# Performance work log

Measured on AMD Instinct MI355X. Metric: run time of the kernel, lower is better.

The kernel has to match this reference:

```python
import jax, jax.numpy as jnp
import numpy as np

NUM_GROUPS = 8
NUM_HEADS = 4
EPS = 1e-5


def group_norm(x, w, b):
    # x: [B, C, H, W]; normalize over (C/G, H, W) within each of G groups
    B, C, H, W = x.shape
    xg = x.reshape(B, NUM_GROUPS, C // NUM_GROUPS, H, W)
    mean = xg.mean(axis=(2, 3, 4), keepdims=True)
    var = xg.var(axis=(2, 3, 4), keepdims=True)
    xn = ((xg - mean) * jax.lax.rsqrt(var + EPS)).reshape(B, C, H, W)
    return xn * w[None, :, None, None] + b[None, :, None, None]


def setup_inputs() -> dict:
    key = jax.random.key(0)
    ks = jax.random.split(key, 7)
    B, C, H, W = 4, 256, 64, 64
    x = jax.random.normal(ks[0], (B, C, H, W), dtype=jnp.float32)
    gn_w = jax.random.normal(ks[1], (C,), dtype=jnp.float32) * 0.1 + 1.0
    gn_b = jax.random.normal(ks[2], (C,), dtype=jnp.float32) * 0.1
    qkv_w = jax.random.normal(ks[3], (3 * C, C), dtype=jnp.float32) / np.sqrt(C)
    qkv_b = jax.random.normal(ks[4], (3 * C,), dtype=jnp.float32) * 0.02
    proj_w = jax.random.normal(ks[5], (C, C), dtype=jnp.float32) / np.sqrt(C)
    proj_b = jax.random.normal(ks[6], (C,), dtype=jnp.float32) * 0.02
    return {"x": x, "gn_w": gn_w, "gn_b": gn_b, "qkv_w": qkv_w,
            "qkv_b": qkv_b, "proj_w": proj_w, "proj_b": proj_b}


def reference(x, gn_w, gn_b, qkv_w, qkv_b, proj_w, proj_b):
    B, C, H, W = x.shape
    nh = NUM_HEADS
    hd = C // nh
    scale = hd ** -0.5
    N = H * W

    h = group_norm(x, gn_w, gn_b)
    # 1x1 conv == channel matmul: [B, 3C, H, W]
    qkv = jnp.einsum('oc,bchw->bohw', qkv_w, h) + qkv_b[None, :, None, None]
    qkv = qkv.reshape(B, 3, nh, hd, N)  # matches torch .view(B,3,nh,hd,HW)
    q, k, v = qkv[:, 0], qkv[:, 1], qkv[:, 2]  # each [B, nh, hd, N]

    attn = jnp.einsum('bhdn,bhdm->bhnm', q, k) * scale  # [B, nh, N, N]
    attn = jax.nn.softmax(attn, axis=-1)
    out = jnp.einsum('bhnm,bhdm->bhdn', attn, v)  # [B, nh, hd, N]
    out = out.reshape(B, C, H, W)

    proj = jnp.einsum('oc,bchw->bohw', proj_w, out) + proj_b[None, :, None, None]
    return x + proj
```

## Files before the change

kernel.cpp:

```cpp
#include <hip/hip_runtime.h>
#include <hip/hip_bf16.h>

#define BB   4
#define CC   256
#define NN   4096
#define NH   4
#define HD   64
#define NG   8
#define GSZ  32
#define EPSV 1e-5f
#define SCALE_L2E 0.18033688f

typedef __bf16 bf16x8 __attribute__((ext_vector_type(8)));
typedef float  f32x4  __attribute__((ext_vector_type(4)));
typedef short  short4v __attribute__((ext_vector_type(4)));

#define MFMA16(a, b, c)  __builtin_amdgcn_mfma_f32_16x16x32_bf16((a), (b), (c), 0, 0, 0)
#define MFMAPV(a, b, c)  __builtin_amdgcn_mfma_f32_16x16x16bf16_1k((a), (b), (c), 0, 0, 0)

#if __has_builtin(__builtin_amdgcn_exp2f)
#define EXP2F __builtin_amdgcn_exp2f
#else
#define EXP2F exp2f
#endif

__device__ inline unsigned short f2bf(float f) {
    unsigned int u = __float_as_uint(f);
    u += 0x7fffu + ((u >> 16) & 1u);
    return (unsigned short)(u >> 16);
}

__device__ __forceinline__ short4v pk4(const f32x4& p) {
    alignas(8) unsigned int u[2];
    u[0] = __builtin_amdgcn_perm(__float_as_uint(p[1]), __float_as_uint(p[0]), 0x07060302u);
    u[1] = __builtin_amdgcn_perm(__float_as_uint(p[3]), __float_as_uint(p[2]), 0x07060302u);
    return *reinterpret_cast<short4v*>(u);
}

__device__ __forceinline__ void async_ld16(void* lds, const void* g) {
    __builtin_amdgcn_global_load_lds(
        (const __attribute__((address_space(1))) unsigned int*)g,
        (__attribute__((address_space(3))) unsigned int*)lds, 16, 0, 0);
}

__global__ void k_prep(const float* __restrict__ x, float* __restrict__ stats,
                       const float* __restrict__ wq, const float* __restrict__ wp,
                       unsigned short* __restrict__ oq, unsigned short* __restrict__ op) {
    int blk = blockIdx.x;
    int t = threadIdx.x;
    if (blk >= 256) {
        int i = (blk - 256) * 256 + t;
        if (i < 3 * CC * CC) oq[i] = f2bf(wq[i]);
        if (i < CC * CC)     op[i] = f2bf(wp[i]);
        return;
    }
    int b = blk >> 6, g = (blk >> 3) & 7, s = blk & 7;
    const float* p = x + ((size_t)(b * CC + g * GSZ)) * NN + s * 16384;
    float s0 = 0.f, s1 = 0.f;
    #pragma unroll
    for (int i = 0; i < 64; ++i) { float v = p[i * 256 + t]; s0 += v; s1 += v * v; }
    #pragma unroll
    for (int m = 1; m <= 32; m <<= 1) { s0 += __shfl_xor(s0, m); s1 += __shfl_xor(s1, m); }
    __shared__ float ls[8];
    int w = t >> 6;
    if ((t & 63) == 0) { ls[w * 2] = s0; ls[w * 2 + 1] = s1; }
    __syncthreads();
    if (t == 0) {
        float a0 = ls[0] + ls[2] + ls[4] + ls[6];
        float a1 = ls[1] + ls[3] + ls[5] + ls[7];
        atomicAdd(&stats[(b * NG + g) * 2 + 0], a0);
        atomicAdd(&stats[(b * NG + g) * 2 + 1], a1);
    }
}

__global__ void k_gnapply(const float* __restrict__ x, const float* __restrict__ gw,
                          const float* __restrict__ gb, const float* __restrict__ stats,
                          unsigned short* __restrict__ ht) {
    int b = blockIdx.z, ct = blockIdx.y, nt = blockIdx.x;
    int c0 = ct * 32, n0 = nt * 64;
    int t = threadIdx.x;
    __shared__ float tile[32][65];
    const float* xp = x + ((size_t)(b * CC + c0)) * NN + n0;
    int cl = t >> 6, nl = t & 63;
    #pragma unroll
    for (int p = 0; p < 8; ++p)
        tile[p * 4 + cl][nl] = xp[(size_t)(p * 4 + cl) * NN + nl];
    float sum = stats[(b * NG + ct) * 2 + 0];
    float ssq = stats[(b * NG + ct) * 2 + 1];
    float mean = sum * (1.0f / 131072.0f);
    float var  = ssq * (1.0f / 131072.0f) - mean * mean;
    float inv  = rsqrtf(var + EPSV);
    __syncthreads();
    int nw = t >> 2, ci = (t & 3) * 8;
    alignas(16) unsigned short o8[8];
    #pragma unroll
    for (int j = 0; j < 8; ++j) {
        int c = c0 + ci + j;
        float v = (tile[ci + j][nw] - mean) * inv * gw[c] + gb[c];
        o8[j] = f2bf(v);
    }
    *reinterpret_cast<uint4*>(ht + ((size_t)(b * NN + n0 + nw)) * CC + c0 + ci) =
        *reinterpret_cast<const uint4*>(o8);
}

__global__ void __launch_bounds__(256)
k_qkv(const unsigned short* __restrict__ ht, const unsigned short* __restrict__ wq,
      const float* __restrict__ qb,
      unsigned short* __restrict__ qt, unsigned short* __restrict__ kt,
      unsigned short* __restrict__ vt) {
    int bx = blockIdx.x, by = blockIdx.y;
    int t = threadIdx.x, wave = t >> 6, lane = t & 63;
    int l15 = lane & 15, quad = lane >> 4;
    int wm = wave >> 1, wn = wave & 1;

    __shared__ alignas(16) unsigned char At[2][8192];
    __shared__ alignas(16) unsigned char Bt[2][8192];

    const char* Ag = (const char*)wq + (size_t)by * 65536;
    const char* Bg = (const char*)ht + (size_t)bx * 65536;
    int row0 = t >> 2, slot = t & 3;
    size_t a0 = (size_t)row0 * 512 + slot * 16;
    size_t a1 = a0 + 64 * 512;
    unsigned int dst0 = wave * 1024;

    auto stage = [&](int buf, int kk) {
        size_t ko = (size_t)kk * 64;
        async_ld16(At[buf] + dst0,        Ag + a0 + ko);
        async_ld16(At[buf] + 4096 + dst0, Ag + a1 + ko);
        async_ld16(Bt[buf] + dst0,        Bg + a0 + ko);
        async_ld16(Bt[buf] + 4096 + dst0, Bg + a1 + ko);
    };

    f32x4 acc[4][4];
    #pragma unroll
    for (int i = 0; i < 4; ++i)
        #pragma unroll
        for (int j = 0; j < 4; ++j) acc[i][j] = (f32x4){0.f, 0.f, 0.f, 0.f};

    stage(0, 0);
    __syncthreads();

    for (int kk = 0; kk < 8; ++kk) {
        int cur = kk & 1;
        if (kk < 7) stage(cur ^ 1, kk + 1);
        bf16x8 af[4], bf[4];
        #pragma unroll
        for (int f = 0; f < 4; ++f) {
            af[f] = *reinterpret_cast<const bf16x8*>(At[cur] + (wm * 64 + f * 16 + l15) * 64 + quad * 16);
            bf[f] = *reinterpret_cast<const bf16x8*>(Bt[cur] + (wn * 64 + f * 16 + l15) * 64 + quad * 16);
        }
        #pragma unroll
        for (int fm = 0; fm < 4; ++fm)
            #pragma unroll
            for (int fn = 0; fn < 4; ++fn)
                acc[fm][fn] = MFMA16(af[fm], bf[fn], acc[fm][fn]);
        __syncthreads();
    }

    int s = by >> 1;
    int nn0 = bx * 128;
    int b = nn0 >> 12, nbase = nn0 & 4095;
    #pragma unroll
    for (int fm = 0; fm < 4; ++fm) {
        int o = by * 128 + wm * 64 + fm * 16 + quad * 4;
        int h = (o >> 6) & 3, d0 = o & 63;
        float bias[4];
        #pragma unroll
        for (int r = 0; r < 4; ++r) bias[r] = qb[o + r];
        #pragma unroll
        for (int fn = 0; fn < 4; ++fn) {
            int n = nbase + wn * 64 + fn * 16 + l15;
            if (s == 0) {
                alignas(8) unsigned short o4[4];
                #pragma unroll
                for (int r = 0; r < 4; ++r) o4[r] = f2bf((acc[fm][fn][r] + bias[r]) * SCALE_L2E);
                *reinterpret_cast<uint2*>(qt + (((size_t)(b * NH + h) * NN) + n) * HD + d0) =
                    *reinterpret_cast<const uint2*>(o4);
            } else if (s == 1) {
                alignas(8) unsigned short o4[4];
                #pragma unroll
                for (int r = 0; r < 4; ++r) o4[r] = f2bf(acc[fm][fn][r] + bias[r]);
                *reinterpret_cast<uint2*>(kt + (((size_t)(b * NH + h) * NN) + n) * HD + d0) =
                    *reinterpret_cast<const uint2*>(o4);
            } else {
                #pragma unroll
                for (int r = 0; r < 4; ++r)
                    vt[((size_t)(b * NH + h) * HD + d0 + r) * NN + n] = f2bf(acc[fm][fn][r] + bias[r]);
            }
        }
    }
}

__global__ void __launch_bounds__(256, 4)
k_attn(const unsigned short* __restrict__ qt, const unsigned short* __restrict__ kt,
       const unsigned short* __restrict__ vt,
       unsigned short* __restrict__ op0, unsigned short* __restrict__ op1,
       float* __restrict__ lip) {
    int bh = blockIdx.y;
    int split = blockIdx.z;
    int t = threadIdx.x, wave = t >> 6, lane = t & 63;
    int l15 = lane & 15, quad = lane >> 4;
    int qbase = blockIdx.x * 128 + wave * 32;
    int kbase = split * 2048;
    const unsigned short* qp = qt + (size_t)bh * NN * HD;
    const unsigned short* kp = kt + (size_t)bh * NN * HD;
    const unsigned short* vp = vt + (size_t)bh * HD * NN;

    __shared__ alignas(16) unsigned char kbuf[2][8192];
    __shared__ alignas(16) unsigned char vbuf[2][8192];

    int lr8 = lane >> 3, lc8 = lane & 7;
    int swz = lc8 ^ lr8;
    const char* ksrc = (const char*)kp + (size_t)(kbase + wave * 16 + lr8) * 128 + swz * 16;
    const char* vsrc = (const char*)vp + (size_t)(wave * 16 + lr8) * 8192 + (size_t)kbase * 2 + swz * 16;
    unsigned int dstw = wave * 2048;

    auto stage = [&](int buf) {
        async_ld16(kbuf[buf] + dstw,        ksrc);
        async_ld16(kbuf[buf] + dstw + 1024, ksrc + 1024);
        ksrc += 8192;
        async_ld16(vbuf[buf] + dstw,        vsrc);
        async_ld16(vbuf[buf] + dstw + 1024, vsrc + 8 * 8192);
        vsrc += 128;
    };

    bf16x8 qaA0 = *reinterpret_cast<const bf16x8*>(qp + (size_t)(qbase + l15) * HD + quad * 8);
    bf16x8 qaA1 = *reinterpret_cast<const bf16x8*>(qp + (size_t)(qbase + l15) * HD + 32 + quad * 8);
    bf16x8 qaB0 = *reinterpret_cast<const bf16x8*>(qp + (size_t)(qbase + 16 + l15) * HD + quad * 8);
    bf16x8 qaB1 = *reinterpret_cast<const bf16x8*>(qp + (size_t)(qbase + 16 + l15) * HD + 32 + quad * 8);

    f32x4 OA[4], OB[4];
    #pragma unroll
    for (int i = 0; i < 4; ++i) { OA[i] = (f32x4){0.f, 0.f, 0.f, 0.f}; OB[i] = (f32x4){0.f, 0.f, 0.f, 0.f}; }
    float liA = 0.f, liB = 0.f;

    int sx = l15 & 7;

    auto compute = [&](const unsigned char* kb, const unsigned char* vbb) {
        #pragma unroll
        for (int s = 0; s < 2; ++s) {
            int r0 = (s * 32 + l15) * 128;
            bf16x8 k00 = *reinterpret_cast<const bf16x8*>(kb + r0 + ((quad ^ sx) * 16));
            bf16x8 k01 = *reinterpret_cast<const bf16x8*>(kb + r0 + (((quad + 4) ^ sx) * 16));
            bf16x8 k10 = *reinterpret_cast<const bf16x8*>(kb + r0 + 2048 + ((quad ^ sx) * 16));
            bf16x8 k11 = *reinterpret_cast<const bf16x8*>(kb + r0 + 2048 + (((quad + 4) ^ sx) * 16));
            f32x4 sA0 = {0.f,0.f,0.f,0.f}, sA1 = {0.f,0.f,0.f,0.f};
            f32x4 sB0 = {0.f,0.f,0.f,0.f}, sB1 = {0.f,0.f,0.f,0.f};
            sA0 = MFMA16(k00, qaA0, sA0);  sA0 = MFMA16(k01, qaA1, sA0);
            sA1 = MFMA16(k10, qaA0, sA1);  sA1 = MFMA16(k11, qaA1, sA1);
            sB0 = MFMA16(k00, qaB0, sB0);  sB0 = MFMA16(k01, qaB1, sB0);
            sB1 = MFMA16(k10, qaB0, sB1);  sB1 = MFMA16(k11, qaB1, sB1);

            f32x4 pA0, pA1, pB0, pB1;
            #pragma unroll
            for (int r = 0; r < 4; ++r) {
                pA0[r] = EXP2F(sA0[r]);  pA1[r] = EXP2F(sA1[r]);
                pB0[r] = EXP2F(sB0[r]);  pB1[r] = EXP2F(sB1[r]);
            }
            liA += (pA0[0] + pA0[1] + pA0[2] + pA0[3]) + (pA1[0] + pA1[1] + pA1[2] + pA1[3]);
            liB += (pB0[0] + pB0[1] + pB0[2] + pB0[3]) + (pB1[0] + pB1[1] + pB1[2] + pB1[3]);

            short4v fA0 = pk4(pA0), fA1 = pk4(pA1), fB0 = pk4(pB0), fB1 = pk4(pB1);

            #pragma unroll
            for (int dc = 0; dc < 4; ++dc) {
                int c0 = ((s * 4 + (quad >> 1)) ^ sx) * 16 + (quad & 1) * 8;
                int c1 = ((s * 4 + 2 + (quad >> 1)) ^ sx) * 16 + (quad & 1) * 8;
                const unsigned char* vrow = vbb + (dc * 16 + l15) * 128;
                short4v v0 = *reinterpret_cast<const short4v*>(vrow + c0);
                short4v v1 = *reinterpret_cast<const short4v*>(vrow + c1);
                OA[dc] = MFMAPV(fA0, v0, OA[dc]);
                OA[dc] = MFMAPV(fA1, v1, OA[dc]);
                OB[dc] = MFMAPV(fB0, v0, OB[dc]);
                OB[dc] = MFMAPV(fB1, v1, OB[dc]);
            }
        }
    };

    stage(0);
    __syncthreads();

    for (int p = 0; p < 16; ++p) {
        stage(1);
        compute(kbuf[0], vbuf[0]);
        __syncthreads();
        if (p < 15) stage(0);
        compute(kbuf[1], vbuf[1]);
        __syncthreads();
    }

    liA += __shfl_xor(liA, 16);  liA += __shfl_xor(liA, 32);
    liB += __shfl_xor(liB, 16);  liB += __shfl_xor(liB, 32);

    unsigned short* op = split ? op1 : op0;
    int b = bh >> 2, h = bh & 3;
    #pragma unroll
    for (int dc = 0; dc < 4; ++dc) {
        #pragma unroll
        for (int r = 0; r < 4; ++r) {
            int qA = qbase + quad * 4 + r;
            op[((size_t)(b * NN) + qA) * CC + h * HD + dc * 16 + l15]      = f2bf(OA[dc][r]);
            op[((size_t)(b * NN) + qA + 16) * CC + h * HD + dc * 16 + l15] = f2bf(OB[dc][r]);
        }
    }
    float* lp = lip + (size_t)split * (16 * NN) + (size_t)bh * NN + qbase;
    if (quad == 0)      lp[l15]      = liA;
    else if (quad == 1) lp[16 + l15] = liB;
}

__global__ void __launch_bounds__(256)
k_comb(unsigned short* ao, const unsigned short* __restrict__ p1, const float* __restrict__ lip) {
    int g = blockIdx.x * 256 + threadIdx.x;
    int d8 = g & 7;
    int h  = (g >> 3) & 3;
    int n  = (g >> 5) & 4095;
    int b  = g >> 17;
    int bh = b * 4 + h;
    float li0 = lip[(size_t)bh * NN + n];
    float li1 = lip[(size_t)16 * NN + (size_t)bh * NN + n];
    float inv = 1.0f / (li0 + li1);
    size_t idx = ((size_t)(b * NN) + n) * CC + h * HD + d8 * 8;
    uint4 u0 = *reinterpret_cast<const uint4*>(ao + idx);
    uint4 u1 = *reinterpret_cast<const uint4*>(p1 + idx);
    const unsigned short* a0 = reinterpret_cast<const unsigned short*>(&u0);
    const unsigned short* a1 = reinterpret_cast<const unsigned short*>(&u1);
    alignas(16) unsigned short o8[8];
    #pragma unroll
    for (int i = 0; i < 8; ++i) {
        float f0 = __uint_as_float((unsigned)a0[i] << 16);
        float f1 = __uint_as_float((unsigned)a1[i] << 16);
        o8[i] = f2bf((f0 + f1) * inv);
    }
    *reinterpret_cast<uint4*>(ao + idx) = *reinterpret_cast<const uint4*>(o8);
}

__global__ void __launch_bounds__(256)
k_proj(const unsigned short* __restrict__ ao, const unsigned short* __restrict__ wp,
       const float* __restrict__ pb, const float* __restrict__ x,
       float* __restrict__ out) {
    int bx = blockIdx.x, by = blockIdx.y;
    int t = threadIdx.x, wave = t >> 6, lane = t & 63;
    int l15 = lane & 15, quad = lane >> 4;
    int wm = wave >> 1, wn = wave & 1;

    __shared__ alignas(16) unsigned char At[2][4096];
    __shared__ alignas(16) unsigned char Bt[2][4096];

    const char* Ag = (const char*)wp + (size_t)by * 32768;
    const char* Bg = (const char*)ao + (size_t)bx * 32768;
    int row0 = t >> 2, slot = t & 3;
    size_t a0 = (size_t)row0 * 512 + slot * 16;
    unsigned int dst0 = wave * 1024;

    auto stage = [&](int buf, int kk) {
        size_t ko = (size_t)kk * 64;
        async_ld16(At[buf] + dst0, Ag + a0 + ko);
        async_ld16(Bt[buf] + dst0, Bg + a0 + ko);
    };

    f32x4 acc[2][2];
    #pragma unroll
    for (int i = 0; i < 2; ++i)
        #pragma unroll
        for (int j = 0; j < 2; ++j) acc[i][j] = (f32x4){0.f, 0.f, 0.f, 0.f};

    stage(0, 0);
    __syncthreads();

    for (int kk = 0; kk < 8; ++kk) {
        int cur = kk & 1;
        if (kk < 7) stage(cur ^ 1, kk + 1);
        bf16x8 af[2], bf[2];
        #pragma unroll
        for (int f = 0; f < 2; ++f) {
            af[f] = *reinterpret_cast<const bf16x8*>(At[cur] + (wm * 32 + f * 16 + l15) * 64 + quad * 16);
            bf[f] = *reinterpret_cast<const bf16x8*>(Bt[cur] + (wn * 32 + f * 16 + l15) * 64 + quad * 16);
        }
        #pragma unroll
        for (int fm = 0; fm < 2; ++fm)
            #pragma unroll
            for (int fn = 0; fn < 2; ++fn)
                acc[fm][fn] = MFMA16(af[fm], bf[fn], acc[fm][fn]);
        __syncthreads();
    }

    int nn0 = bx * 64;
    int b = nn0 >> 12, nbase = nn0 & 4095;
    #pragma unroll
    for (int fm = 0; fm < 2; ++fm) {
        int o = by * 64 + wm * 32 + fm * 16 + quad * 4;
        float bias[4];
        #pragma unroll
        for (int r = 0; r < 4; ++r) bias[r] = pb[o + r];
        #pragma unroll
        for (int fn = 0; fn < 2; ++fn) {
            int n = nbase + wn * 32 + fn * 16 + l15;
            #pragma unroll
            for (int r = 0; r < 4; ++r) {
                size_t idx = ((size_t)(b * CC + o + r)) * NN + n;
                out[idx] = acc[fm][fn][r] + bias[r] + x[idx];
            }
        }
    }
}

extern "C" void kernel_launch(void* const* d_in, const int* in_sizes, int n_in,
                              void* d_out, int out_size, void* d_ws, size_t ws_size,
                              hipStream_t stream) {
    const float* x     = (const float*)d_in[0];
    const float* gw    = (const float*)d_in[1];
    const float* gb    = (const float*)d_in[2];
    const float* qkvw  = (const float*)d_in[3];
    const float* qkvb  = (const float*)d_in[4];
    const float* projw = (const float*)d_in[5];
    const float* projb = (const float*)d_in[6];
    float* out = (float*)d_out;

    char* w = (char*)d_ws;
    size_t off = 0;
    unsigned short* ht = (unsigned short*)(w + off); off += (size_t)BB * NN * CC * 2;
    unsigned short* qt = (unsigned short*)(w + off); off += (size_t)BB * NH * NN * HD * 2;
    unsigned short* kt = (unsigned short*)(w + off); off += (size_t)BB * NH * NN * HD * 2;
    unsigned short* vt = (unsigned short*)(w + off); off += (size_t)BB * NH * HD * NN * 2;
    unsigned short* ao = (unsigned short*)(w + off); off += (size_t)BB * NN * CC * 2;
    unsigned short* wqb = (unsigned short*)(w + off); off += (size_t)3 * CC * CC * 2;
    unsigned short* wpb = (unsigned short*)(w + off); off += (size_t)CC * CC * 2;
    float* stats = (float*)(w + off); off += BB * NG * 2 * sizeof(float);
    float* lip   = (float*)(w + off); off += (size_t)2 * 16 * NN * sizeof(float);

    hipMemsetAsync(stats, 0, BB * NG * 2 * sizeof(float), stream);
    k_prep<<<1024, 256, 0, stream>>>(x, stats, qkvw, projw, wqb, wpb);
    k_gnapply<<<dim3(NN / 64, CC / 32, BB), 256, 0, stream>>>(x, gw, gb, stats, ht);
    k_qkv<<<dim3(BB * NN / 128, 6), 256, 0, stream>>>(ht, wqb, qkvb, qt, kt, vt);
    k_attn<<<dim3(NN / 128, BB * NH, 2), 256, 0, stream>>>(qt, kt, vt, ao, ht, lip);
    k_comb<<<2048, 256, 0, stream>>>(ao, ht, lip);
    k_proj<<<dim3(BB * NN / 64, CC / 64), 256, 0, stream>>>(ao, wpb, projb, x, out);
}
```

Before: 199.2 us.

## Fuse split-attention combine into projection GEMM and batch QK MFMAs before exp

Removes the separate k_comb kernel. The projection kernel now loads both partial attention outputs from global memory, sums them, scales by the inverse softmax denominator and writes the bf16 result into shared memory as its B operand. This saves a kernel launch and one full read-write pass over the attention output, but each of the CC/64 column blocks now redoes the combine and reads two inputs instead of one. The attention inner loop also issues all QK MFMAs for both sub-steps before the exponentials, giving the scheduler more independent MFMA work at the cost of more live registers.

Result: no change. 200.2 us (+0.5%).

```diff
diff --git a/kernel.cpp b/kernel.cpp
--- a/kernel.cpp
+++ b/kernel.cpp
@@ -237,6 +237,7 @@
     int sx = l15 & 7;
 
     auto compute = [&](const unsigned char* kb, const unsigned char* vbb) {
+        f32x4 sA0[2], sA1[2], sB0[2], sB1[2];
         #pragma unroll
         for (int s = 0; s < 2; ++s) {
             int r0 = (s * 32 + l15) * 128;
@@ -244,18 +245,20 @@
             bf16x8 k01 = *reinterpret_cast<const bf16x8*>(kb + r0 + (((quad + 4) ^ sx) * 16));
             bf16x8 k10 = *reinterpret_cast<const bf16x8*>(kb + r0 + 2048 + ((quad ^ sx) * 16));
             bf16x8 k11 = *reinterpret_cast<const bf16x8*>(kb + r0 + 2048 + (((quad + 4) ^ sx) * 16));
-            f32x4 sA0 = {0.f,0.f,0.f,0.f}, sA1 = {0.f,0.f,0.f,0.f};
-            f32x4 sB0 = {0.f,0.f,0.f,0.f}, sB1 = {0.f,0.f,0.f,0.f};
-            sA0 = MFMA16(k00, qaA0, sA0);  sA0 = MFMA16(k01, qaA1, sA0);
-            sA1 = MFMA16(k10, qaA0, sA1);  sA1 = MFMA16(k11, qaA1, sA1);
-            sB0 = MFMA16(k00, qaB0, sB0);  sB0 = MFMA16(k01, qaB1, sB0);
-            sB1 = MFMA16(k10, qaB0, sB1);  sB1 = MFMA16(k11, qaB1, sB1);
-
+            sA0[s] = (f32x4){0.f,0.f,0.f,0.f};  sA1[s] = (f32x4){0.f,0.f,0.f,0.f};
+            sB0[s] = (f32x4){0.f,0.f,0.f,0.f};  sB1[s] = (f32x4){0.f,0.f,0.f,0.f};
+            sA0[s] = MFMA16(k00, qaA0, sA0[s]);  sA0[s] = MFMA16(k01, qaA1, sA0[s]);
+            sA1[s] = MFMA16(k10, qaA0, sA1[s]);  sA1[s] = MFMA16(k11, qaA1, sA1[s]);
+            sB0[s] = MFMA16(k00, qaB0, sB0[s]);  sB0[s] = MFMA16(k01, qaB1, sB0[s]);
+            sB1[s] = MFMA16(k10, qaB0, sB1[s]);  sB1[s] = MFMA16(k11, qaB1, sB1[s]);
+        }
+        #pragma unroll
+        for (int s = 0; s < 2; ++s) {
             f32x4 pA0, pA1, pB0, pB1;
             #pragma unroll
             for (int r = 0; r < 4; ++r) {
-                pA0[r] = EXP2F(sA0[r]);  pA1[r] = EXP2F(sA1[r]);
-                pB0[r] = EXP2F(sB0[r]);  pB1[r] = EXP2F(sB1[r]);
+                pA0[r] = EXP2F(sA0[s][r]);  pA1[r] = EXP2F(sA1[s][r]);
+                pB0[r] = EXP2F(sB0[s][r]);  pB1[r] = EXP2F(sB1[s][r]);
             }
             liA += (pA0[0] + pA0[1] + pA0[2] + pA0[3]) + (pA1[0] + pA1[1] + pA1[2] + pA1[3]);
             liB += (pB0[0] + pB0[1] + pB0[2] + pB0[3]) + (pB1[0] + pB1[1] + pB1[2] + pB1[3]);
@@ -309,35 +312,10 @@
 }
 
 __global__ void __launch_bounds__(256)
-k_comb(unsigned short* ao, const unsigned short* __restrict__ p1, const float* __restrict__ lip) {
-    int g = blockIdx.x * 256 + threadIdx.x;
-    int d8 = g & 7;
-    int h  = (g >> 3) & 3;
-    int n  = (g >> 5) & 4095;
-    int b  = g >> 17;
-    int bh = b * 4 + h;
-    float li0 = lip[(size_t)bh * NN + n];
-    float li1 = lip[(size_t)16 * NN + (size_t)bh * NN + n];
-    float inv = 1.0f / (li0 + li1);
-    size_t idx = ((size_t)(b * NN) + n) * CC + h * HD + d8 * 8;
-    uint4 u0 = *reinterpret_cast<const uint4*>(ao + idx);
-    uint4 u1 = *reinterpret_cast<const uint4*>(p1 + idx);
-    const unsigned short* a0 = reinterpret_cast<const unsigned short*>(&u0);
-    const unsigned short* a1 = reinterpret_cast<const unsigned short*>(&u1);
-    alignas(16) unsigned short o8[8];
-    #pragma unroll
-    for (int i = 0; i < 8; ++i) {
-        float f0 = __uint_as_float((unsigned)a0[i] << 16);
-        float f1 = __uint_as_float((unsigned)a1[i] << 16);
-        o8[i] = f2bf((f0 + f1) * inv);
-    }
-    *reinterpret_cast<uint4*>(ao + idx) = *reinterpret_cast<const uint4*>(o8);
-}
-
-__global__ void __launch_bounds__(256)
-k_proj(const unsigned short* __restrict__ ao, const unsigned short* __restrict__ wp,
-       const float* __restrict__ pb, const float* __restrict__ x,
-       float* __restrict__ out) {
+k_proj(const unsigned short* __restrict__ p0, const unsigned short* __restrict__ p1,
+       const float* __restrict__ lip,
+       const unsigned short* __restrict__ wp, const float* __restrict__ pb,
+       const float* __restrict__ x, float* __restrict__ out) {
     int bx = blockIdx.x, by = blockIdx.y;
     int t = threadIdx.x, wave = t >> 6, lane = t & 63;
     int l15 = lane & 15, quad = lane >> 4;
@@ -347,15 +325,44 @@
     __shared__ alignas(16) unsigned char Bt[2][4096];
 
     const char* Ag = (const char*)wp + (size_t)by * 32768;
-    const char* Bg = (const char*)ao + (size_t)bx * 32768;
     int row0 = t >> 2, slot = t & 3;
     size_t a0 = (size_t)row0 * 512 + slot * 16;
     unsigned int dst0 = wave * 1024;
 
-    auto stage = [&](int buf, int kk) {
-        size_t ko = (size_t)kk * 64;
-        async_ld16(At[buf] + dst0, Ag + a0 + ko);
-        async_ld16(Bt[buf] + dst0, Bg + a0 + ko);
+    int nn0 = bx * 64;
+    int b = nn0 >> 12, nbase = nn0 & 4095;
+    int myn = nbase + row0;
+    float inv[4];
+    #pragma unroll
+    for (int h = 0; h < 4; ++h) {
+        int bh = b * 4 + h;
+        float li0 = lip[(size_t)bh * NN + myn];
+        float li1 = lip[(size_t)16 * NN + (size_t)bh * NN + myn];
+        inv[h] = 1.0f / (li0 + li1);
+    }
+    size_t brow = ((size_t)(b * NN) + myn) * CC + slot * 8;
+
+    auto stageA = [&](int buf, int kk) {
+        async_ld16(At[buf] + dst0, Ag + a0 + (size_t)kk * 64);
+    };
+    auto loadB = [&](int kk, uint4& u0, uint4& u1) {
+        size_t idx = brow + kk * 32;
+        u0 = *reinterpret_cast<const uint4*>(p0 + idx);
+        u1 = *reinterpret_cast<const uint4*>(p1 + idx);
+    };
+    auto writeB = [&](int buf, int kk, const uint4& u0, const uint4& u1) {
+        float iv = inv[kk >> 1];
+        const unsigned short* a0p = reinterpret_cast<const unsigned short*>(&u0);
+        const unsigned short* a1p = reinterpret_cast<const unsigned short*>(&u1);
+        alignas(16) unsigned short o8[8];
+        #pragma unroll
+        for (int i = 0; i < 8; ++i) {
+            float f0 = __uint_as_float((unsigned)a0p[i] << 16);
+            float f1 = __uint_as_float((unsigned)a1p[i] << 16);
+            o8[i] = f2bf((f0 + f1) * iv);
+        }
+        *reinterpret_cast<uint4*>(Bt[buf] + row0 * 64 + slot * 16) =
+            *reinterpret_cast<const uint4*>(o8);
     };
 
     f32x4 acc[2][2];
@@ -364,12 +371,21 @@
         #pragma unroll
         for (int j = 0; j < 2; ++j) acc[i][j] = (f32x4){0.f, 0.f, 0.f, 0.f};
 
-    stage(0, 0);
+    {
+        uint4 u0, u1;
+        loadB(0, u0, u1);
+        stageA(0, 0);
+        writeB(0, 0, u0, u1);
+    }
     __syncthreads();
 
     for (int kk = 0; kk < 8; ++kk) {
         int cur = kk & 1;
-        if (kk < 7) stage(cur ^ 1, kk + 1);
+        uint4 u0, u1;
+        if (kk < 7) {
+            loadB(kk + 1, u0, u1);
+            stageA(cur ^ 1, kk + 1);
+        }
         bf16x8 af[2], bf[2];
         #pragma unroll
         for (int f = 0; f < 2; ++f) {
@@ -381,11 +397,10 @@
             #pragma unroll
             for (int fn = 0; fn < 2; ++fn)
                 acc[fm][fn] = MFMA16(af[fm], bf[fn], acc[fm][fn]);
+        if (kk < 7) writeB(cur ^ 1, kk + 1, u0, u1);
         __syncthreads();
     }
 
-    int nn0 = bx * 64;
-    int b = nn0 >> 12, nbase = nn0 & 4095;
     #pragma unroll
     for (int fm = 0; fm < 2; ++fm) {
         int o = by * 64 + wm * 32 + fm * 16 + quad * 4;
@@ -433,6 +448,5 @@
     k_gnapply<<<dim3(NN / 64, CC / 32, BB), 256, 0, stream>>>(x, gw, gb, stats, ht);
     k_qkv<<<dim3(BB * NN / 128, 6), 256, 0, stream>>>(ht, wqb, qkvb, qt, kt, vt);
     k_attn<<<dim3(NN / 128, BB * NH, 2), 256, 0, stream>>>(qt, kt, vt, ao, ht, lip);
-    k_comb<<<2048, 256, 0, stream>>>(ao, ht, lip);
-    k_proj<<<dim3(BB * NN / 64, CC / 64), 256, 0, stream>>>(ao, wpb, projb, x, out);
-}
+    k_proj<<<dim3(BB * NN / 64, CC / 64), 256, 0, stream>>>(ao, ht, lip, wpb, projb, x, out);
+}
```
